# Kernel optimization log

Hardware: AMD Instinct MI355X
Metric: run time of the kernel (lower is better)

## Reference

```python
import jax, jax.numpy as jnp
import numpy as np

B, S, H, N, D, R = 2, 2048, 768, 12, 64, 5  # batch, seq, hidden, heads, head_dim, n_structural_deps


def setup_inputs() -> dict:
    key = jax.random.key(0)
    ks = jax.random.split(key, 12)
    hidden_states = jax.random.normal(ks[0], (B, S, H), dtype=jnp.float32)
    attention_mask = jnp.zeros((B, 1, 1, S), dtype=jnp.float32)  # additive mask, all-visible
    # binary structural adjacency per dependency, broadcast over heads
    graph_adj = (jax.random.uniform(ks[1], (R, B, 1, S, S)) < 0.1).astype(jnp.float32)
    s = 0.02
    Wq = jax.random.normal(ks[2], (H, H), dtype=jnp.float32) * s
    bq = jnp.zeros((H,), dtype=jnp.float32)
    Wk = jax.random.normal(ks[3], (H, H), dtype=jnp.float32) * s
    bk = jnp.zeros((H,), dtype=jnp.float32)
    Wv = jax.random.normal(ks[4], (H, H), dtype=jnp.float32) * s
    bv = jnp.zeros((H,), dtype=jnp.float32)
    # biaffine bilinear forms, one [N, D, D] per structural dependency
    bili = jax.random.normal(ks[5], (R, N, D, D), dtype=jnp.float32) * s
    abs_bias = jnp.zeros((R, N), dtype=jnp.float32)  # initialized to zeros as in torch
    return {
        'hidden_states': hidden_states, 'attention_mask': attention_mask,
        'graph_adj': graph_adj, 'Wq': Wq, 'bq': bq, 'Wk': Wk, 'bk': bk,
        'Wv': Wv, 'bv': bv, 'bili': bili, 'abs_bias': abs_bias, 'layer_idx': 0,
    }


def reference(hidden_states, attention_mask, graph_adj, Wq, bq, Wk, bk, Wv, bv,
              bili, abs_bias, layer_idx):
    b, s, h = hidden_states.shape
    n, d = N, D

    def heads(x):  # [b, s, h] -> [b, n, s, d]
        return x.reshape(b, s, n, d).transpose(0, 2, 1, 3)

    q = heads(hidden_states @ Wq.T + bq)
    k = heads(hidden_states @ Wk.T + bk)
    v = heads(hidden_states @ Wv.T + bv)

    scores = jnp.einsum('bnid,bnjd->bnij', q, k)  # [b, n, s, s]
    # biaffine structural bias per dependency, masked by graph adjacency
    for i in range(R):  # small fixed structural loop
        bias = jnp.einsum('bnip,npq,bnjq->bnij', q, bili[i], k)
        bias = bias + abs_bias[i][None, :, None, None]
        scores = scores + bias * graph_adj[i]

    scores = scores / np.sqrt(d).astype(np.float32) + attention_mask
    probs = jax.nn.softmax(scores, axis=-1)
    ctx = jnp.einsum('bnij,bnjd->bnid', probs, v)  # [b, n, s, d]
    return ctx.transpose(0, 2, 1, 3).reshape(b, s, h)
```

## Files before the change

### kernel.cpp

```cpp
#include <hip/hip_runtime.h>
#include <cstdint>
#include <cstddef>

#define B_  2
#define S_  2048
#define H_  768
#define NH  12
#define DH  64
#define RD  5
#define BN  (B_*NH)

typedef _Float16 f16;
typedef __attribute__((ext_vector_type(8))) _Float16 f16x8;
typedef __attribute__((ext_vector_type(4))) float f32x4;

#define MFMA16(a, b, c) __builtin_amdgcn_mfma_f32_16x16x32_f16((a), (b), (c), 0, 0, 0)

#if __has_builtin(__builtin_amdgcn_exp2f)
__device__ __forceinline__ float exp2fast(float x) { return __builtin_amdgcn_exp2f(x); }
#else
__device__ __forceinline__ float exp2fast(float x) { return __expf(0.69314718056f * x); }
#endif

#define SCL 0.1803368801f
#define L2E 1.44269504f

#define NX4 ((B_*S_*H_)/4)
#define NW4 ((H_*H_)/4)

__global__ __launch_bounds__(256) void cvtall(
    const float* __restrict__ x,
    const float* __restrict__ wq, const float* __restrict__ wk,
    const float* __restrict__ wv,
    f16* __restrict__ xh, f16* __restrict__ wh)
{
    int idx = blockIdx.x * 256 + threadIdx.x;
    const int total4 = NX4 + 3 * NW4;
    if (idx >= total4) return;
    const float* src;
    f16* dst;
    int off;
    if (idx < NX4) {
        src = x; dst = xh; off = idx;
    } else {
        int r = idx - NX4;
        int which = r / NW4;
        off = r - which * NW4;
        src = (which == 0) ? wq : (which == 1) ? wk : wv;
        dst = wh + (size_t)which * H_ * H_;
    }
    float4 f = ((const float4*)src)[off];
    f16 h[4] = {(f16)f.x, (f16)f.y, (f16)f.z, (f16)f.w};
    ((ushort4*)dst)[off] = *(const ushort4*)h;
}

__global__ __launch_bounds__(256, 3) void qkv_gemm(
    const f16* __restrict__ xh, const f16* __restrict__ wh,
    const float* __restrict__ bq, const float* __restrict__ bk,
    const float* __restrict__ bv,
    f16* __restrict__ qo, f16* __restrict__ ko, f16* __restrict__ vt)
{
    __shared__ __align__(16) f16 Xs[64][72];
    __shared__ __align__(16) f16 Ws[3][64][72];

    const int tid = threadIdx.x;
    const int n  = blockIdx.x;
    const int m0 = blockIdx.y * 64;
    const int w = tid >> 6, lane = tid & 63;
    const int l15 = lane & 15, quad = lane >> 4;
    const int srow = tid >> 2, sc0 = (tid & 3) * 16;

    f32x4 acc[3][4];
#pragma unroll
    for (int i = 0; i < 3; ++i)
#pragma unroll
        for (int ns = 0; ns < 4; ++ns) acc[i][ns] = (f32x4){0.f, 0.f, 0.f, 0.f};

    const f16* xsrc = xh + (size_t)(m0 + srow) * H_ + sc0;
    const f16* wsrc = wh + (size_t)(n * 64 + srow) * H_ + sc0;

    for (int kc = 0; kc < 12; ++kc) {
        __syncthreads();
        {
            const f16* s0 = xsrc + kc * 64;
            *(f16x8*)&Xs[srow][sc0]     = *(const f16x8*)(s0);
            *(f16x8*)&Xs[srow][sc0 + 8] = *(const f16x8*)(s0 + 8);
        }
#pragma unroll
        for (int i = 0; i < 3; ++i) {
            const f16* s0 = wsrc + (size_t)i * H_ * H_ + kc * 64;
            *(f16x8*)&Ws[i][srow][sc0]     = *(const f16x8*)(s0);
            *(f16x8*)&Ws[i][srow][sc0 + 8] = *(const f16x8*)(s0 + 8);
        }
        __syncthreads();

        f16x8 a0 = *(const f16x8*)&Xs[w * 16 + l15][quad * 8];
        f16x8 a1 = *(const f16x8*)&Xs[w * 16 + l15][quad * 8 + 32];
#pragma unroll
        for (int i = 0; i < 3; ++i)
#pragma unroll
            for (int ns = 0; ns < 4; ++ns) {
                f16x8 b0 = *(const f16x8*)&Ws[i][ns * 16 + l15][quad * 8];
                f16x8 b1 = *(const f16x8*)&Ws[i][ns * 16 + l15][quad * 8 + 32];
                acc[i][ns] = MFMA16(a0, b0, acc[i][ns]);
                acc[i][ns] = MFMA16(a1, b1, acc[i][ns]);
            }
    }
    __syncthreads();

    const float* bias[3] = {bq, bk, bv};
    f16 (*T0)[72] = Xs;
    f16 (*T1)[72] = Ws[0];
    f16 (*T2)[72] = Ws[1];
#pragma unroll
    for (int i = 0; i < 3; ++i) {
        f16 (*T)[72] = (i == 0) ? T0 : (i == 1) ? T1 : T2;
#pragma unroll
        for (int ns = 0; ns < 4; ++ns) {
            float bb = bias[i][n * 64 + ns * 16 + l15];
#pragma unroll
            for (int reg = 0; reg < 4; ++reg)
                T[w * 16 + quad * 4 + reg][ns * 16 + l15] =
                    (f16)(acc[i][ns][reg] + bb);
        }
    }
    __syncthreads();

    const int mrow = m0 + srow;
    const int bb2 = mrow >> 11, ss = mrow & 2047;
    {
        f16* dst = qo + ((size_t)(bb2 * NH + n) * S_ + ss) * DH + sc0;
        *(f16x8*)dst       = *(const f16x8*)&T0[srow][sc0];
        *(f16x8*)(dst + 8) = *(const f16x8*)&T0[srow][sc0 + 8];
    }
    {
        f16* dst = ko + ((size_t)(bb2 * NH + n) * S_ + ss) * DH + sc0;
        *(f16x8*)dst       = *(const f16x8*)&T1[srow][sc0];
        *(f16x8*)(dst + 8) = *(const f16x8*)&T1[srow][sc0 + 8];
    }
    {
        f16 tmp[16];
#pragma unroll
        for (int u = 0; u < 16; ++u) tmp[u] = T2[sc0 + u][srow];
        f16* dst = vt + ((size_t)(bb2 * NH + n) * DH + srow) * S_ + (m0 & 2047) + sc0;
        *(f16x8*)dst       = *(const f16x8*)&tmp[0];
        *(f16x8*)(dst + 8) = *(const f16x8*)&tmp[8];
    }
}

__global__ __launch_bounds__(256) void adjpack(
    const float* __restrict__ adj, unsigned char* __restrict__ adjp)
{
    const int idx4 = blockIdx.x * 256 + threadIdx.x;
    const int j4 = idx4 & 511;
    const int iq = (idx4 >> 9) & 511;
    const int b  = idx4 >> 18;
    unsigned int wbits[4] = {0, 0, 0, 0};
#pragma unroll
    for (int r = 0; r < RD; ++r) {
#pragma unroll
        for (int ii = 0; ii < 4; ++ii) {
            float4 v = *(const float4*)(adj +
                (((size_t)(r * B_ + b) * S_) + iq * 4 + ii) * S_ + j4 * 4);
            float vv[4] = {v.x, v.y, v.z, v.w};
#pragma unroll
            for (int jj = 0; jj < 4; ++jj)
                wbits[jj] |= (vv[jj] != 0.f ? 1u : 0u) << (r + 8 * ii);
        }
    }
    uint4 pk = {wbits[0], wbits[1], wbits[2], wbits[3]};
    *(uint4*)(adjp + ((size_t)(b * 512 + iq) * S_ + j4 * 4) * 4) = pk;
}

__global__ __launch_bounds__(256, 3) void attn(
    const f16* __restrict__ q, const f16* __restrict__ k, const f16* __restrict__ vt,
    const float* __restrict__ bili, const unsigned char* __restrict__ adjp,
    const float* __restrict__ mask, const float* __restrict__ absb,
    float* __restrict__ out)
{
    __shared__ __align__(16) char smem[9216 + 9216 + 128];
    f16*   Mt  = (f16*)smem;
    f16*   Pb  = (f16*)(smem + 9216);
    float* lut = (float*)(smem + 9216 + 9216);

    const int tid = threadIdx.x;
    const int idx = blockIdx.x;
    const int g = idx & 7;
    const int it = (idx >> 3) & 31;
    const int bn = 8 * (idx >> 8) + g;
    const int b = bn / NH, n = bn % NH;
    const int w = tid >> 6, lane = tid & 63;
    const int l15 = lane & 15, quad = lane >> 4;
    const int wi0 = it * 64 + w * 16;
    const size_t kbase = (size_t)bn * S_ * DH;

    if (tid < 32) {
        float a = 0.f;
#pragma unroll
        for (int r = 0; r < RD; ++r)
            if (tid & (1 << r)) a += absb[r * NH + n];
        lut[tid] = a * SCL;
    }

    const f16* qrow = q + kbase + (size_t)(wi0 + l15) * DH + quad * 8;
    f16x8 aq0 = *(const f16x8*)(qrow);
    f16x8 aq1 = *(const f16x8*)(qrow + 32);

    f16* Pw = Pb + w * 16 * 72;

    f16x8 aqp[RD][2];
#pragma unroll
    for (int r = 0; r < RD; ++r) {
        __syncthreads();
        {
            int p = tid >> 2, q0 = (tid & 3) * 16;
            const float* src = bili + ((size_t)(r * NH + n) * DH + p) * DH + q0;
            float4 g0 = ((const float4*)src)[0];
            float4 g1 = ((const float4*)src)[1];
            float4 g2 = ((const float4*)src)[2];
            float4 g3 = ((const float4*)src)[3];
            float mv[16] = {g0.x, g0.y, g0.z, g0.w, g1.x, g1.y, g1.z, g1.w,
                            g2.x, g2.y, g2.z, g2.w, g3.x, g3.y, g3.z, g3.w};
#pragma unroll
            for (int u = 0; u < 16; ++u) Mt[(q0 + u) * 72 + p] = (f16)mv[u];
        }
        __syncthreads();
#pragma unroll
        for (int ns = 0; ns < 4; ++ns) {
            f16x8 b0 = *(const f16x8*)&Mt[(ns * 16 + l15) * 72 + quad * 8];
            f16x8 b1 = *(const f16x8*)&Mt[(ns * 16 + l15) * 72 + quad * 8 + 32];
            f32x4 d = {0.f, 0.f, 0.f, 0.f};
            d = MFMA16(aq0, b0, d);
            d = MFMA16(aq1, b1, d);
#pragma unroll
            for (int reg = 0; reg < 4; ++reg)
                Pw[(quad * 4 + reg) * 72 + ns * 16 + l15] = (f16)d[reg];
        }
        aqp[r][0] = *(const f16x8*)&Pw[l15 * 72 + quad * 8];
        aqp[r][1] = *(const f16x8*)&Pw[l15 * 72 + quad * 8 + 32];
    }

    f16x8 ones;
#pragma unroll
    for (int u = 0; u < 8; ++u) ones[u] = (f16)1.0f;

    f32x4 o[4] = {{0,0,0,0},{0,0,0,0},{0,0,0,0},{0,0,0,0}};
    f32x4 lacc = {0.f, 0.f, 0.f, 0.f};
    float mrun[4] = {-1e30f, -1e30f, -1e30f, -1e30f};

    const unsigned char* adjrow =
        adjp + (size_t)(b * 512 + (wi0 >> 2) + quad) * (S_ * 4);
    const float* maskrow = mask + (size_t)b * S_;
    const f16* vtb = vt + (size_t)bn * DH * S_;

    f16x8 kb0a, kb0b, kb1a, kb1b, kb2a, kb2b, kb3a, kb3b;
    f16x8 vb0a, vb0b, vb1a, vb1b, vb2a, vb2b, vb3a, vb3b;

#define LOAD_KB(T) do {                                                      \
    const f16* kp_ = k + kbase + (size_t)((T) * 64 + l15) * DH + quad * 8;   \
    kb0a = *(const f16x8*)(kp_);                                             \
    kb0b = *(const f16x8*)(kp_ + 32);                                        \
    kb1a = *(const f16x8*)(kp_ + 16 * DH);                                   \
    kb1b = *(const f16x8*)(kp_ + 16 * DH + 32);                              \
    kb2a = *(const f16x8*)(kp_ + 32 * DH);                                   \
    kb2b = *(const f16x8*)(kp_ + 32 * DH + 32);                              \
    kb3a = *(const f16x8*)(kp_ + 48 * DH);                                   \
    kb3b = *(const f16x8*)(kp_ + 48 * DH + 32);                              \
} while (0)

#define LOAD_VB(T) do {                                                      \
    const f16* vp_ = vtb + (size_t)l15 * S_ + (T) * 64 + quad * 8;           \
    vb0a = *(const f16x8*)(vp_);                                             \
    vb0b = *(const f16x8*)(vp_ + 32);                                        \
    vb1a = *(const f16x8*)(vp_ + 16 * S_);                                   \
    vb1b = *(const f16x8*)(vp_ + 16 * S_ + 32);                              \
    vb2a = *(const f16x8*)(vp_ + 32 * S_);                                   \
    vb2b = *(const f16x8*)(vp_ + 32 * S_ + 32);                              \
    vb3a = *(const f16x8*)(vp_ + 48 * S_);                                   \
    vb3b = *(const f16x8*)(vp_ + 48 * S_ + 32);                              \
} while (0)

#define SCORE1(T, JS, KA, KB_, O0, O1, O2, O3) do {                          \
    const int jcol_ = (T) * 64 + (JS) * 16 + l15;                            \
    f32x4 aqk_ = {0.f, 0.f, 0.f, 0.f};                                       \
    aqk_ = MFMA16(aq0, KA, aqk_);                                            \
    aqk_ = MFMA16(aq1, KB_, aqk_);                                           \
    uchar4 a4_ = *(const uchar4*)(adjrow + (size_t)jcol_ * 4);               \
    unsigned int c0_ = a4_.x, c1_ = a4_.y, c2_ = a4_.z, c3_ = a4_.w;         \
    float mkL_ = maskrow[jcol_] * L2E;                                       \
    float t0_ = aqk_[0], t1_ = aqk_[1], t2_ = aqk_[2], t3_ = aqk_[3];        \
    _Pragma("unroll")                                                        \
    for (int r = 0; r < RD; ++r) {                                           \
        f32x4 z_ = {0.f, 0.f, 0.f, 0.f};                                     \
        z_ = MFMA16(aqp[r][0], KA, z_);                                      \
        z_ = MFMA16(aqp[r][1], KB_, z_);                                     \
        t0_ = fmaf((float)((c0_ >> r) & 1u), z_[0], t0_);                    \
        t1_ = fmaf((float)((c1_ >> r) & 1u), z_[1], t1_);                    \
        t2_ = fmaf((float)((c2_ >> r) & 1u), z_[2], t2_);                    \
        t3_ = fmaf((float)((c3_ >> r) & 1u), z_[3], t3_);                    \
    }                                                                        \
    O0 = fmaf(t0_, SCL, lut[c0_] + mkL_);                                    \
    O1 = fmaf(t1_, SCL, lut[c1_] + mkL_);                                    \
    O2 = fmaf(t2_, SCL, lut[c2_] + mkL_);                                    \
    O3 = fmaf(t3_, SCL, lut[c3_] + mkL_);                                    \
} while (0)

    LOAD_KB(0);

#pragma unroll 1
    for (int t = 0; t < 32; ++t) {
        const int j0 = t * 64;

        LOAD_VB(t);

        float sc[4][4];
        SCORE1(t, 0, kb0a, kb0b, sc[0][0], sc[0][1], sc[0][2], sc[0][3]);
        SCORE1(t, 1, kb1a, kb1b, sc[1][0], sc[1][1], sc[1][2], sc[1][3]);
        SCORE1(t, 2, kb2a, kb2b, sc[2][0], sc[2][1], sc[2][2], sc[2][3]);
        SCORE1(t, 3, kb3a, kb3b, sc[3][0], sc[3][1], sc[3][2], sc[3][3]);

        {
            int tn = t + 1;
            if (tn > 31) tn = 31;
            LOAD_KB(tn);
        }

        float alpha[4];
#pragma unroll
        for (int reg = 0; reg < 4; ++reg) {
            float nm = fmaxf(fmaxf(sc[0][reg], sc[1][reg]),
                             fmaxf(sc[2][reg], sc[3][reg]));
#pragma unroll
            for (int off = 1; off < 16; off <<= 1)
                nm = fmaxf(nm, __shfl_xor(nm, off));
            float mn = fmaxf(mrun[reg], nm);
            alpha[reg] = exp2fast(mrun[reg] - mn);
            mrun[reg] = mn;
        }
#pragma unroll
        for (int js = 0; js < 4; ++js)
#pragma unroll
            for (int reg = 0; reg < 4; ++reg) {
                float p = exp2fast(sc[js][reg] - mrun[reg]);
                Pw[(quad * 4 + reg) * 72 + js * 16 + l15] = (f16)p;
            }
#pragma unroll
        for (int reg = 0; reg < 4; ++reg) {
            lacc[reg] *= alpha[reg];
#pragma unroll
            for (int ds = 0; ds < 4; ++ds) o[ds][reg] *= alpha[reg];
        }

        f16x8 pa0 = *(const f16x8*)&Pw[l15 * 72 + quad * 8];
        f16x8 pa1 = *(const f16x8*)&Pw[l15 * 72 + quad * 8 + 32];
        lacc = MFMA16(pa0, ones, lacc);
        lacc = MFMA16(pa1, ones, lacc);
        o[0] = MFMA16(pa0, vb0a, o[0]);
        o[0] = MFMA16(pa1, vb0b, o[0]);
        o[1] = MFMA16(pa0, vb1a, o[1]);
        o[1] = MFMA16(pa1, vb1b, o[1]);
        o[2] = MFMA16(pa0, vb2a, o[2]);
        o[2] = MFMA16(pa1, vb2b, o[2]);
        o[3] = MFMA16(pa0, vb3a, o[3]);
        o[3] = MFMA16(pa1, vb3b, o[3]);
    }

#undef SCORE1
#undef LOAD_KB
#undef LOAD_VB

#pragma unroll
    for (int reg = 0; reg < 4; ++reg) {
        float inv = 1.f / lacc[reg];
        int i = wi0 + quad * 4 + reg;
#pragma unroll
        for (int ds = 0; ds < 4; ++ds)
            out[((size_t)b * S_ + i) * H_ + n * DH + ds * 16 + l15] =
                o[ds][reg] * inv;
    }
}

extern "C" void kernel_launch(void* const* d_in, const int* in_sizes, int n_in,
                              void* d_out, int out_size, void* d_ws, size_t ws_size,
                              hipStream_t stream)
{
    const float* hs   = (const float*)d_in[0];
    const float* mask = (const float*)d_in[1];
    const float* adj  = (const float*)d_in[2];
    const float* Wq   = (const float*)d_in[3];
    const float* bq   = (const float*)d_in[4];
    const float* Wk   = (const float*)d_in[5];
    const float* bk   = (const float*)d_in[6];
    const float* Wv   = (const float*)d_in[7];
    const float* bv   = (const float*)d_in[8];
    const float* bili = (const float*)d_in[9];
    const float* absb = (const float*)d_in[10];
    float* out = (float*)d_out;

    const size_t QKV = (size_t)BN * S_ * DH;
    f16* q  = (f16*)d_ws;
    f16* k  = q + QKV;
    f16* vt = k + QKV;
    unsigned char* adjp = (unsigned char*)(vt + QKV);
    f16* xh = (f16*)(adjp + (size_t)B_ * 512 * S_ * 4);
    f16* wh = xh + (size_t)B_ * S_ * H_;

    const int total4 = NX4 + 3 * NW4;
    cvtall<<<(total4 + 255) / 256, 256, 0, stream>>>(hs, Wq, Wk, Wv, xh, wh);
    qkv_gemm<<<dim3(12, 64), 256, 0, stream>>>(xh, wh, bq, bk, bv, q, k, vt);
    adjpack<<<2048, 256, 0, stream>>>(adj, adjp);
    attn<<<768, 256, 0, stream>>>(q, k, vt, bili, adjp, mask, absb, out);
}
```

Measured before the change: 506.2 us.

## Merge QKV GEMM with adjacency packing and add lazy softmax rescaling

The QKV projection GEMM and the adjacency bit-packing kernel now run as one launch, with block indices at 768 and above doing the packing. This removes a kernel boundary and lets the GEMM and the bandwidth-bound packing share the GPU. In the attention loop the online-softmax max reduction, the rescale exponent and the accumulator rescale are skipped when every lane's new tile maximum stays within 8 (log2 units) of the running maximum. In that case the exponentials are taken against a stale maximum, which can grow up to 2^8 before fp16 conversion and slightly changes the rounding behaviour.

```diff
diff --git a/kernel.cpp b/kernel.cpp
--- a/kernel.cpp
+++ b/kernel.cpp
@@ -54,18 +54,43 @@
     ((ushort4*)dst)[off] = *(const ushort4*)h;
 }
 
-__global__ __launch_bounds__(256, 3) void qkv_gemm(
+__global__ __launch_bounds__(256, 3) void qkv_pack(
     const f16* __restrict__ xh, const f16* __restrict__ wh,
     const float* __restrict__ bq, const float* __restrict__ bk,
     const float* __restrict__ bv,
-    f16* __restrict__ qo, f16* __restrict__ ko, f16* __restrict__ vt)
+    f16* __restrict__ qo, f16* __restrict__ ko, f16* __restrict__ vt,
+    const float* __restrict__ adj, unsigned char* __restrict__ adjp)
 {
     __shared__ __align__(16) f16 Xs[64][72];
     __shared__ __align__(16) f16 Ws[3][64][72];
 
     const int tid = threadIdx.x;
-    const int n  = blockIdx.x;
-    const int m0 = blockIdx.y * 64;
+
+    if (blockIdx.x >= 768) {
+        const int idx4 = (blockIdx.x - 768) * 256 + tid;
+        const int j4 = idx4 & 511;
+        const int iq = (idx4 >> 9) & 511;
+        const int b  = idx4 >> 18;
+        unsigned int wbits[4] = {0, 0, 0, 0};
+#pragma unroll
+        for (int r = 0; r < RD; ++r) {
+#pragma unroll
+            for (int ii = 0; ii < 4; ++ii) {
+                float4 v = *(const float4*)(adj +
+                    (((size_t)(r * B_ + b) * S_) + iq * 4 + ii) * S_ + j4 * 4);
+                float vv[4] = {v.x, v.y, v.z, v.w};
+#pragma unroll
+                for (int jj = 0; jj < 4; ++jj)
+                    wbits[jj] |= (vv[jj] != 0.f ? 1u : 0u) << (r + 8 * ii);
+            }
+        }
+        uint4 pk = {wbits[0], wbits[1], wbits[2], wbits[3]};
+        *(uint4*)(adjp + ((size_t)(b * 512 + iq) * S_ + j4 * 4) * 4) = pk;
+        return;
+    }
+
+    const int n  = blockIdx.x % 12;
+    const int m0 = (blockIdx.x / 12) * 64;
     const int w = tid >> 6, lane = tid & 63;
     const int l15 = lane & 15, quad = lane >> 4;
     const int srow = tid >> 2, sc0 = (tid & 3) * 16;
@@ -146,30 +171,6 @@
         *(f16x8*)dst       = *(const f16x8*)&tmp[0];
         *(f16x8*)(dst + 8) = *(const f16x8*)&tmp[8];
     }
-}
-
-__global__ __launch_bounds__(256) void adjpack(
-    const float* __restrict__ adj, unsigned char* __restrict__ adjp)
-{
-    const int idx4 = blockIdx.x * 256 + threadIdx.x;
-    const int j4 = idx4 & 511;
-    const int iq = (idx4 >> 9) & 511;
-    const int b  = idx4 >> 18;
-    unsigned int wbits[4] = {0, 0, 0, 0};
-#pragma unroll
-    for (int r = 0; r < RD; ++r) {
-#pragma unroll
-        for (int ii = 0; ii < 4; ++ii) {
-            float4 v = *(const float4*)(adj +
-                (((size_t)(r * B_ + b) * S_) + iq * 4 + ii) * S_ + j4 * 4);
-            float vv[4] = {v.x, v.y, v.z, v.w};
-#pragma unroll
-            for (int jj = 0; jj < 4; ++jj)
-                wbits[jj] |= (vv[jj] != 0.f ? 1u : 0u) << (r + 8 * ii);
-        }
-    }
-    uint4 pk = {wbits[0], wbits[1], wbits[2], wbits[3]};
-    *(uint4*)(adjp + ((size_t)(b * 512 + iq) * S_ + j4 * 4) * 4) = pk;
 }
 
 __global__ __launch_bounds__(256, 3) void attn(
@@ -325,17 +326,29 @@
             LOAD_KB(tn);
         }
 
-        float alpha[4];
-#pragma unroll
-        for (int reg = 0; reg < 4; ++reg) {
-            float nm = fmaxf(fmaxf(sc[0][reg], sc[1][reg]),
-                             fmaxf(sc[2][reg], sc[3][reg]));
-#pragma unroll
-            for (int off = 1; off < 16; off <<= 1)
-                nm = fmaxf(nm, __shfl_xor(nm, off));
-            float mn = fmaxf(mrun[reg], nm);
-            alpha[reg] = exp2fast(mrun[reg] - mn);
-            mrun[reg] = mn;
+        float lm[4];
+#pragma unroll
+        for (int reg = 0; reg < 4; ++reg)
+            lm[reg] = fmaxf(fmaxf(sc[0][reg], sc[1][reg]),
+                            fmaxf(sc[2][reg], sc[3][reg]));
+        bool ok = true;
+#pragma unroll
+        for (int reg = 0; reg < 4; ++reg)
+            ok = ok && (lm[reg] <= mrun[reg] + 8.0f);
+        if (!__all(ok)) {
+#pragma unroll
+            for (int reg = 0; reg < 4; ++reg) {
+                float nm = lm[reg];
+#pragma unroll
+                for (int off = 1; off < 16; off <<= 1)
+                    nm = fmaxf(nm, __shfl_xor(nm, off));
+                float mn = fmaxf(mrun[reg], nm);
+                float alpha = exp2fast(mrun[reg] - mn);
+                mrun[reg] = mn;
+                lacc[reg] *= alpha;
+#pragma unroll
+                for (int ds = 0; ds < 4; ++ds) o[ds][reg] *= alpha;
+            }
         }
 #pragma unroll
         for (int js = 0; js < 4; ++js)
@@ -344,12 +357,6 @@
                 float p = exp2fast(sc[js][reg] - mrun[reg]);
                 Pw[(quad * 4 + reg) * 72 + js * 16 + l15] = (f16)p;
             }
-#pragma unroll
-        for (int reg = 0; reg < 4; ++reg) {
-            lacc[reg] *= alpha[reg];
-#pragma unroll
-            for (int ds = 0; ds < 4; ++ds) o[ds][reg] *= alpha[reg];
-        }
 
         f16x8 pa0 = *(const f16x8*)&Pw[l15 * 72 + quad * 8];
         f16x8 pa1 = *(const f16x8*)&Pw[l15 * 72 + quad * 8 + 32];
@@ -407,7 +414,7 @@
 
     const int total4 = NX4 + 3 * NW4;
     cvtall<<<(total4 + 255) / 256, 256, 0, stream>>>(hs, Wq, Wk, Wv, xh, wh);
-    qkv_gemm<<<dim3(12, 64), 256, 0, stream>>>(xh, wh, bq, bk, bv, q, k, vt);
-    adjpack<<<2048, 256, 0, stream>>>(adj, adjp);
+    qkv_pack<<<768 + 2048, 256, 0, stream>>>(xh, wh, bq, bk, bv,
+                                             q, k, vt, adj, adjp);
     attn<<<768, 256, 0, stream>>>(q, k, vt, bili, adjp, mask, absb, out);
 }
```

After: 543.0 us. +7.3%, slower.

## Fuse fp16 conversion into QKV GEMM and merge adjacency packing into one launch

Applied to the files above, without the earlier changes.

Drops the separate fp32-to-fp16 conversion kernel: the QKV GEMM now reads fp32 activations and weights directly and converts them while staging into shared memory. The adjacency bit-packing kernel becomes extra blocks of the same launch, so two kernel launches and the fp16 intermediate round trip through global memory go away, and packing can overlap with the GEMM. In exchange the GEMM loads twice the bytes per tile from global memory, and the combined kernel's launch bounds and register budget now also apply to the packing blocks.

```diff
diff --git a/kernel.cpp b/kernel.cpp
--- a/kernel.cpp
+++ b/kernel.cpp
@@ -25,47 +25,59 @@
 #define SCL 0.1803368801f
 #define L2E 1.44269504f
 
-#define NX4 ((B_*S_*H_)/4)
-#define NW4 ((H_*H_)/4)
-
-__global__ __launch_bounds__(256) void cvtall(
-    const float* __restrict__ x,
-    const float* __restrict__ wq, const float* __restrict__ wk,
-    const float* __restrict__ wv,
-    f16* __restrict__ xh, f16* __restrict__ wh)
+__device__ __forceinline__ void cvt16(const float* __restrict__ src, f16* dst)
 {
-    int idx = blockIdx.x * 256 + threadIdx.x;
-    const int total4 = NX4 + 3 * NW4;
-    if (idx >= total4) return;
-    const float* src;
-    f16* dst;
-    int off;
-    if (idx < NX4) {
-        src = x; dst = xh; off = idx;
-    } else {
-        int r = idx - NX4;
-        int which = r / NW4;
-        off = r - which * NW4;
-        src = (which == 0) ? wq : (which == 1) ? wk : wv;
-        dst = wh + (size_t)which * H_ * H_;
-    }
-    float4 f = ((const float4*)src)[off];
-    f16 h[4] = {(f16)f.x, (f16)f.y, (f16)f.z, (f16)f.w};
-    ((ushort4*)dst)[off] = *(const ushort4*)h;
+    float4 f0 = ((const float4*)src)[0];
+    float4 f1 = ((const float4*)src)[1];
+    float4 f2 = ((const float4*)src)[2];
+    float4 f3 = ((const float4*)src)[3];
+    f16 h[16] = {(f16)f0.x, (f16)f0.y, (f16)f0.z, (f16)f0.w,
+                 (f16)f1.x, (f16)f1.y, (f16)f1.z, (f16)f1.w,
+                 (f16)f2.x, (f16)f2.y, (f16)f2.z, (f16)f2.w,
+                 (f16)f3.x, (f16)f3.y, (f16)f3.z, (f16)f3.w};
+    *(f16x8*)dst       = *(const f16x8*)&h[0];
+    *(f16x8*)(dst + 8) = *(const f16x8*)&h[8];
 }
 
-__global__ __launch_bounds__(256, 3) void qkv_gemm(
-    const f16* __restrict__ xh, const f16* __restrict__ wh,
+__global__ __launch_bounds__(256, 3) void qkv_pack(
+    const float* __restrict__ hs,
+    const float* __restrict__ Wq, const float* __restrict__ Wk,
+    const float* __restrict__ Wv,
     const float* __restrict__ bq, const float* __restrict__ bk,
     const float* __restrict__ bv,
-    f16* __restrict__ qo, f16* __restrict__ ko, f16* __restrict__ vt)
+    f16* __restrict__ qo, f16* __restrict__ ko, f16* __restrict__ vt,
+    const float* __restrict__ adj, unsigned char* __restrict__ adjp)
 {
     __shared__ __align__(16) f16 Xs[64][72];
     __shared__ __align__(16) f16 Ws[3][64][72];
 
     const int tid = threadIdx.x;
-    const int n  = blockIdx.x;
-    const int m0 = blockIdx.y * 64;
+
+    if (blockIdx.x >= 768) {
+        const int idx4 = (blockIdx.x - 768) * 256 + tid;
+        const int j4 = idx4 & 511;
+        const int iq = (idx4 >> 9) & 511;
+        const int b  = idx4 >> 18;
+        unsigned int wbits[4] = {0, 0, 0, 0};
+#pragma unroll
+        for (int r = 0; r < RD; ++r) {
+#pragma unroll
+            for (int ii = 0; ii < 4; ++ii) {
+                float4 v = *(const float4*)(adj +
+                    (((size_t)(r * B_ + b) * S_) + iq * 4 + ii) * S_ + j4 * 4);
+                float vv[4] = {v.x, v.y, v.z, v.w};
+#pragma unroll
+                for (int jj = 0; jj < 4; ++jj)
+                    wbits[jj] |= (vv[jj] != 0.f ? 1u : 0u) << (r + 8 * ii);
+            }
+        }
+        uint4 pk = {wbits[0], wbits[1], wbits[2], wbits[3]};
+        *(uint4*)(adjp + ((size_t)(b * 512 + iq) * S_ + j4 * 4) * 4) = pk;
+        return;
+    }
+
+    const int n  = blockIdx.x % 12;
+    const int m0 = (blockIdx.x / 12) * 64;
     const int w = tid >> 6, lane = tid & 63;
     const int l15 = lane & 15, quad = lane >> 4;
     const int srow = tid >> 2, sc0 = (tid & 3) * 16;
@@ -76,22 +88,17 @@
 #pragma unroll
         for (int ns = 0; ns < 4; ++ns) acc[i][ns] = (f32x4){0.f, 0.f, 0.f, 0.f};
 
-    const f16* xsrc = xh + (size_t)(m0 + srow) * H_ + sc0;
-    const f16* wsrc = wh + (size_t)(n * 64 + srow) * H_ + sc0;
+    const float* xsrc = hs + (size_t)(m0 + srow) * H_ + sc0;
+    const float* w0src = Wq + (size_t)(n * 64 + srow) * H_ + sc0;
+    const float* w1src = Wk + (size_t)(n * 64 + srow) * H_ + sc0;
+    const float* w2src = Wv + (size_t)(n * 64 + srow) * H_ + sc0;
 
     for (int kc = 0; kc < 12; ++kc) {
         __syncthreads();
-        {
-            const f16* s0 = xsrc + kc * 64;
-            *(f16x8*)&Xs[srow][sc0]     = *(const f16x8*)(s0);
-            *(f16x8*)&Xs[srow][sc0 + 8] = *(const f16x8*)(s0 + 8);
-        }
-#pragma unroll
-        for (int i = 0; i < 3; ++i) {
-            const f16* s0 = wsrc + (size_t)i * H_ * H_ + kc * 64;
-            *(f16x8*)&Ws[i][srow][sc0]     = *(const f16x8*)(s0);
-            *(f16x8*)&Ws[i][srow][sc0 + 8] = *(const f16x8*)(s0 + 8);
-        }
+        cvt16(xsrc  + kc * 64, &Xs[srow][sc0]);
+        cvt16(w0src + kc * 64, &Ws[0][srow][sc0]);
+        cvt16(w1src + kc * 64, &Ws[1][srow][sc0]);
+        cvt16(w2src + kc * 64, &Ws[2][srow][sc0]);
         __syncthreads();
 
         f16x8 a0 = *(const f16x8*)&Xs[w * 16 + l15][quad * 8];
@@ -146,30 +153,6 @@
         *(f16x8*)dst       = *(const f16x8*)&tmp[0];
         *(f16x8*)(dst + 8) = *(const f16x8*)&tmp[8];
     }
-}
-
-__global__ __launch_bounds__(256) void adjpack(
-    const float* __restrict__ adj, unsigned char* __restrict__ adjp)
-{
-    const int idx4 = blockIdx.x * 256 + threadIdx.x;
-    const int j4 = idx4 & 511;
-    const int iq = (idx4 >> 9) & 511;
-    const int b  = idx4 >> 18;
-    unsigned int wbits[4] = {0, 0, 0, 0};
-#pragma unroll
-    for (int r = 0; r < RD; ++r) {
-#pragma unroll
-        for (int ii = 0; ii < 4; ++ii) {
-            float4 v = *(const float4*)(adj +
-                (((size_t)(r * B_ + b) * S_) + iq * 4 + ii) * S_ + j4 * 4);
-            float vv[4] = {v.x, v.y, v.z, v.w};
-#pragma unroll
-            for (int jj = 0; jj < 4; ++jj)
-                wbits[jj] |= (vv[jj] != 0.f ? 1u : 0u) << (r + 8 * ii);
-        }
-    }
-    uint4 pk = {wbits[0], wbits[1], wbits[2], wbits[3]};
-    *(uint4*)(adjp + ((size_t)(b * 512 + iq) * S_ + j4 * 4) * 4) = pk;
 }
 
 __global__ __launch_bounds__(256, 3) void attn(
@@ -402,12 +385,8 @@
     f16* k  = q + QKV;
     f16* vt = k + QKV;
     unsigned char* adjp = (unsigned char*)(vt + QKV);
-    f16* xh = (f16*)(adjp + (size_t)B_ * 512 * S_ * 4);
-    f16* wh = xh + (size_t)B_ * S_ * H_;
-
-    const int total4 = NX4 + 3 * NW4;
-    cvtall<<<(total4 + 255) / 256, 256, 0, stream>>>(hs, Wq, Wk, Wv, xh, wh);
-    qkv_gemm<<<dim3(12, 64), 256, 0, stream>>>(xh, wh, bq, bk, bv, q, k, vt);
-    adjpack<<<2048, 256, 0, stream>>>(adj, adjp);
+
+    qkv_pack<<<768 + 2048, 256, 0, stream>>>(hs, Wq, Wk, Wv, bq, bk, bv,
+                                             q, k, vt, adj, adjp);
     attn<<<768, 256, 0, stream>>>(q, k, vt, bili, adjp, mask, absb, out);
 }
```

Result: faster. 479.4 us, median of 4 (-5.3%).
